# Performance work log

Measured on AMD Instinct MI355X. Metric: run time of the kernel, lower is better.

The kernel has to match this reference:

```python
import jax, jax.numpy as jnp
import numpy as np

B, C, H, W = 32, 256, 56, 56
O, K = 512, 3


def setup_inputs() -> dict:
    key = jax.random.key(0)
    kx, kw = jax.random.split(key)
    x = jax.random.normal(kx, (B, C, H, W), dtype=jnp.float32)
    # Ternary weight stored as two disjoint boolean masks of shape (C*K*K, O),
    # matching the torch buffer layout: weight.view(O, C*K*K).t().
    u = jax.random.uniform(kw, (C * K * K, O))
    pos_weight = u < 0.45
    neg_weight = u > 0.55
    return {"x": x, "pos_weight": pos_weight, "neg_weight": neg_weight}


def reference(x, pos_weight, neg_weight):
    # pos/neg masks: (C*K*K, O) bool, disjoint. The torch module computes
    # sum(unfold(x) where pos) - sum(unfold(x) where neg) over the C*K*K axis
    # per output channel, i.e. a conv with ternary weight in {-1, 0, +1}.
    b, c, h, w = x.shape
    ckk, o = pos_weight.shape
    k = int(round((ckk // c) ** 0.5))  # kernel size (square)
    wt = pos_weight.astype(x.dtype) - neg_weight.astype(x.dtype)  # (C*K*K, O)
    # torch unfold orders the patch axis as (C, kh, kw); weight came from
    # view(O, C*K*K).t(), so transposing back gives OIHW layout directly.
    wt = wt.T.reshape(o, c, k, k)
    pad = (k - 1) // 2  # 'same' padding (output reshaped to (b, O, h, w))
    out = jax.lax.conv_general_dilated(
        x, wt,
        window_strides=(1, 1),
        padding=[(pad, pad), (pad, pad)],
        dimension_numbers=("NCHW", "OIHW", "NCHW"),
    )
    return out  # (b, O, h, w)
```

## Files before the change

kernel.cpp:

```cpp
#include <hip/hip_runtime.h>
#include <hip/hip_bf16.h>

#define BB 32
#define CC 256
#define HH 56
#define WW 56
#define OO 512
#define CKK 2304

#define PROWS 58
#define PPITCH 64
#define PSLICE (PROWS * PPITCH)

#define NY 4
#define NX 28
#define NTILE 112
#define BPITCH 40

typedef __bf16 bf16x8 __attribute__((ext_vector_type(8)));
typedef float  f32x4  __attribute__((ext_vector_type(4)));
typedef unsigned short u16x8 __attribute__((ext_vector_type(8)));

#define WT_OFF 4096
#define XP_OFF (WT_OFF + (size_t)OO * CKK * 2)

__global__ void detect_bool_width(const unsigned int* __restrict__ pos,
                                  unsigned int* __restrict__ flag) {
    unsigned int v = 0;
    for (int i = threadIdx.x; i < 16384; i += 256) v |= pos[i];
    __shared__ unsigned int red;
    if (threadIdx.x == 0) red = 0u;
    __syncthreads();
    if (v > 1u) atomicOr(&red, 1u);
    __syncthreads();
    if (threadIdx.x == 0) *flag = red;
}

__global__ __launch_bounds__(256) void decode_w(
    const void* __restrict__ posv, const void* __restrict__ negv,
    const unsigned int* __restrict__ flag,
    unsigned short* __restrict__ wt) {
    __shared__ unsigned short lds[64][65];
    int blk = blockIdx.x;
    int ot  = blk & 7;
    int khw = (blk >> 3) % 9;
    int ct  = blk / 72;
    int o0 = ot * 64, c0 = ct * 64;
    int t = threadIdx.x;
    int o_l = t & 63, row4 = t >> 6;
    bool bytes = (*flag != 0u);
#pragma unroll
    for (int r = 0; r < 16; ++r) {
        int c_l = row4 + r * 4;
        long k = (long)(c0 + c_l) * 9 + khw;
        long idx = k * OO + o0 + o_l;
        int p, q;
        if (bytes) { p = ((const unsigned char*)posv)[idx];
                     q = ((const unsigned char*)negv)[idx]; }
        else       { p = ((const int*)posv)[idx];
                     q = ((const int*)negv)[idx]; }
        lds[c_l][o_l] = p ? 0x3F80u : (q ? 0xBF80u : 0u);
    }
    __syncthreads();
#pragma unroll
    for (int r = 0; r < 16; ++r) {
        int o_r = row4 + r * 4;
        int kcol = t & 63;
        wt[(size_t)(o0 + o_r) * CKK + khw * 256 + c0 + kcol] = lds[kcol][o_r];
    }
}

__global__ __launch_bounds__(256) void pad_x(const float* __restrict__ x,
                                             unsigned short* __restrict__ xp) {
    int bc = blockIdx.x;
    const float* xs = x + (size_t)bc * (HH * WW);
    unsigned short* xd = xp + (size_t)bc * PSLICE;
    for (int i = threadIdx.x; i < PSLICE; i += 256) {
        int xx = i & 63, yy = i >> 6;
        float v = 0.f;
        if (yy >= 1 && yy <= HH && xx >= 1 && xx <= WW)
            v = xs[(yy - 1) * WW + xx - 1];
        __hip_bfloat16 h = __float2bfloat16(v);
        xd[i] = *(unsigned short*)&h;
    }
}

__global__ __launch_bounds__(256, 2) void conv_mfma(
    const unsigned short* __restrict__ xp,
    const unsigned short* __restrict__ wt,
    float* __restrict__ out) {
    __shared__ __align__(16) unsigned short Bs[NTILE * BPITCH];

    int t = threadIdx.x;
    int w = t >> 6, lane = t & 63, lm = lane & 15, lq = lane >> 4;

    int gn = blockIdx.x;
    int obase = blockIdx.y << 8;
    int b = gn / 28;
    int rem = gn - b * 28;
    int y0 = (rem >> 1) * NY;
    int x0 = (rem & 1) * NX;

    int sn = t % NTILE;
    int ch = t / NTILE;
    bool active = (t < 2 * NTILE);
    int ny = sn / NX, nx = sn - (sn / NX) * NX;
    const unsigned short* xbase =
        xp + (size_t)(b * CC) * PSLICE + (y0 + ny) * PPITCH + (x0 + nx);
    int woff = sn * BPITCH + ch * 16;

    const unsigned short* abase =
        wt + (size_t)(obase + w * 64 + lm) * CKK + lq * 8;

    f32x4 acc[4][7];
#pragma unroll
    for (int i = 0; i < 4; ++i)
#pragma unroll
        for (int j = 0; j < 7; ++j) acc[i][j] = (f32x4){0.f, 0.f, 0.f, 0.f};

    for (int s = 0; s < 72; ++s) {
        int khw = s >> 3;
        int kh = khw / 3, kw = khw - kh * 3;
        int c0 = (s & 7) << 5;

        __syncthreads();
        if (active) {
            const unsigned short* src =
                xbase + (size_t)(c0 + ch * 16) * PSLICE + kh * PPITCH + kw;
            u16x8 v0, v1;
#pragma unroll
            for (int j = 0; j < 8; ++j) v0[j] = src[j * PSLICE];
#pragma unroll
            for (int j = 0; j < 8; ++j) v1[j] = src[(j + 8) * PSLICE];
            *(u16x8*)&Bs[woff] = v0;
            *(u16x8*)&Bs[woff + 8] = v1;
        }
        __syncthreads();

        bf16x8 af[4];
#pragma unroll
        for (int mt = 0; mt < 4; ++mt)
            af[mt] = *(const bf16x8*)(abase + (size_t)mt * 16 * CKK + s * 32);

#pragma unroll
        for (int nt = 0; nt < 7; ++nt) {
            bf16x8 bfr = *(const bf16x8*)&Bs[(nt * 16 + lm) * BPITCH + lq * 8];
#pragma unroll
            for (int mt = 0; mt < 4; ++mt)
                acc[mt][nt] = __builtin_amdgcn_mfma_f32_16x16x32_bf16(
                    af[mt], bfr, acc[mt][nt], 0, 0, 0);
        }
    }

    int orow0 = obase + w * 64 + lq * 4;
#pragma unroll
    for (int mt = 0; mt < 4; ++mt) {
#pragma unroll
        for (int nt = 0; nt < 7; ++nt) {
            int nl = nt * 16 + lm;
            int nyy = nl / NX, nxx = nl - nyy * NX;
            size_t base =
                ((size_t)(b * OO + orow0 + mt * 16) * HH + (y0 + nyy)) * WW +
                (x0 + nxx);
#pragma unroll
            for (int r = 0; r < 4; ++r)
                out[base + (size_t)r * HH * WW] = acc[mt][nt][r];
        }
    }
}

extern "C" void kernel_launch(void* const* d_in, const int* in_sizes, int n_in,
                              void* d_out, int out_size, void* d_ws, size_t ws_size,
                              hipStream_t stream) {
    const float* x   = (const float*)d_in[0];
    const void*  pos = d_in[1];
    const void*  neg = d_in[2];
    float* out = (float*)d_out;

    unsigned int* flag = (unsigned int*)d_ws;
    unsigned short* wt = (unsigned short*)((char*)d_ws + WT_OFF);
    unsigned short* xpad = (unsigned short*)((char*)d_ws + XP_OFF);

    detect_bool_width<<<1, 256, 0, stream>>>((const unsigned int*)pos, flag);
    decode_w<<<288, 256, 0, stream>>>(pos, neg, flag, wt);
    pad_x<<<BB * CC, 256, 0, stream>>>(x, xpad);
    conv_mfma<<<dim3(896, 2), 256, 0, stream>>>(xpad, wt, out);
}
```

Baseline: 759.5 us.

## Switch to channels-last padded input with halo tile staged via direct global-to-LDS loads

The padded input moves from per-channel planes (NCHW) to a channels-last layout (B, 58, 58, C), and the weights are reordered so each 32-channel chunk holds all 9 kernel taps together. The conv kernel now stages one 6x30-pixel halo tile of 32 channels into LDS once, using global_load_lds, and reuses it for all 9 taps. The old kernel gathered strided scalars from global memory for every tap. Staging is double-buffered so the next chunk's copy overlaps the MFMA work, and blocks are remapped so the two output-channel halves of a tile run close together for L2 reuse. The pad kernel gains an LDS transpose, and the conv kernel uses more registers (12 A fragments) and 32KB of LDS.

Result: faster. 616.3 us (-18.9%).

```diff
diff --git a/kernel.cpp b/kernel.cpp
--- a/kernel.cpp
+++ b/kernel.cpp
@@ -8,18 +8,19 @@
 #define OO 512
 #define CKK 2304
 
-#define PROWS 58
-#define PPITCH 64
-#define PSLICE (PROWS * PPITCH)
+#define XR 58
+#define XC 58
+#define XPIX (XR * XC)
 
 #define NY 4
 #define NX 28
 #define NTILE 112
-#define BPITCH 40
+#define TPC 30
+#define TPIX 180
+#define BUFB 16384
 
 typedef __bf16 bf16x8 __attribute__((ext_vector_type(8)));
 typedef float  f32x4  __attribute__((ext_vector_type(4)));
-typedef unsigned short u16x8 __attribute__((ext_vector_type(8)));
 
 #define WT_OFF 4096
 #define XP_OFF (WT_OFF + (size_t)OO * CKK * 2)
@@ -65,23 +66,44 @@
 #pragma unroll
     for (int r = 0; r < 16; ++r) {
         int o_r = row4 + r * 4;
-        int kcol = t & 63;
-        wt[(size_t)(o0 + o_r) * CKK + khw * 256 + c0 + kcol] = lds[kcol][o_r];
+        int c = c0 + (t & 63);
+        wt[(size_t)(o0 + o_r) * CKK + (c >> 5) * 288 + khw * 32 + (c & 31)] =
+            lds[t & 63][o_r];
     }
 }
 
 __global__ __launch_bounds__(256) void pad_x(const float* __restrict__ x,
                                              unsigned short* __restrict__ xp) {
-    int bc = blockIdx.x;
-    const float* xs = x + (size_t)bc * (HH * WW);
-    unsigned short* xd = xp + (size_t)bc * PSLICE;
-    for (int i = threadIdx.x; i < PSLICE; i += 256) {
-        int xx = i & 63, yy = i >> 6;
-        float v = 0.f;
-        if (yy >= 1 && yy <= HH && xx >= 1 && xx <= WW)
-            v = xs[(yy - 1) * WW + xx - 1];
-        __hip_bfloat16 h = __float2bfloat16(v);
-        xd[i] = *(unsigned short*)&h;
+    int blk = blockIdx.x;
+    int b = blk / XR, y = blk - b * XR;
+    int t = threadIdx.x;
+    unsigned short* rowp = xp + ((size_t)b * XPIX + (size_t)y * XC) * CC;
+    if (y == 0 || y == XR - 1) {
+        uint4 z = {0, 0, 0, 0};
+        for (int i = t; i < XC * CC / 8; i += 256) ((uint4*)rowp)[i] = z;
+        return;
+    }
+    __shared__ float lds[WW][65];
+    for (int cb = 0; cb < 4; ++cb) {
+        if (cb) __syncthreads();
+#pragma unroll
+        for (int i = 0; i < 14; ++i) {
+            int idx = i * 256 + t;
+            int cl = idx / WW, xx = idx - cl * WW;
+            lds[xx][cl] =
+                x[(((size_t)b * CC + cb * 64 + cl) * HH + (y - 1)) * WW + xx];
+        }
+        __syncthreads();
+#pragma unroll
+        for (int i = 0; i < 15; ++i) {
+            int idx = i * 256 + t;
+            if (idx < XC * 64) {
+                int xx = idx >> 6, cl = idx & 63;
+                float v = (xx == 0 || xx == XC - 1) ? 0.f : lds[xx - 1][cl];
+                __hip_bfloat16 h = __float2bfloat16(v);
+                rowp[(size_t)xx * CC + cb * 64 + cl] = *(unsigned short*)&h;
+            }
+        }
     }
 }
 
@@ -89,28 +111,44 @@
     const unsigned short* __restrict__ xp,
     const unsigned short* __restrict__ wt,
     float* __restrict__ out) {
-    __shared__ __align__(16) unsigned short Bs[NTILE * BPITCH];
+    __shared__ __align__(1024) unsigned short Bs[2 * BUFB / 2];
 
     int t = threadIdx.x;
     int w = t >> 6, lane = t & 63, lm = lane & 15, lq = lane >> 4;
 
-    int gn = blockIdx.x;
-    int obase = blockIdx.y << 8;
+    int bx = blockIdx.x;
+    int mb = (bx >> 3) & 1;
+    int gn = ((bx >> 4) << 3) | (bx & 7);
     int b = gn / 28;
     int rem = gn - b * 28;
-    int y0 = (rem >> 1) * NY;
+    int y0 = (rem >> 1) << 2;
     int x0 = (rem & 1) * NX;
 
-    int sn = t % NTILE;
-    int ch = t / NTILE;
-    bool active = (t < 2 * NTILE);
-    int ny = sn / NX, nx = sn - (sn / NX) * NX;
-    const unsigned short* xbase =
-        xp + (size_t)(b * CC) * PSLICE + (y0 + ny) * PPITCH + (x0 + nx);
-    int woff = sn * BPITCH + ch * 16;
-
-    const unsigned short* abase =
-        wt + (size_t)(obase + w * 64 + lm) * CKK + lq * 8;
+    int bofs[7];
+#pragma unroll
+    for (int nt = 0; nt < 7; ++nt) {
+        int n = nt * 16 + lm;
+        int ny = n / NX, nx = n - (n / NX) * NX;
+        bofs[nt] = (ny * TPC + nx) * 64 + lq * 16;
+    }
+
+    const unsigned short* gsrc[3];
+    int useg[3];
+#pragma unroll
+    for (int i = 0; i < 3; ++i) {
+        int u = (w * 3 + i) * 64 + lane;
+        useg[i] = u;
+        int pix = u >> 2, quad = u & 3;
+        int py = pix / TPC, px = pix - py * TPC;
+        gsrc[i] = xp + ((size_t)b * XPIX + (y0 + py) * XC + (x0 + px)) * CC +
+                  quad * 8;
+    }
+    int ldsseg = (w * 3) * 1024;
+
+    const unsigned short* aptr[4];
+#pragma unroll
+    for (int mt = 0; mt < 4; ++mt)
+        aptr[mt] = wt + (size_t)(mb * 256 + w * 64 + mt * 16 + lm) * CKK + lq * 8;
 
     f32x4 acc[4][7];
 #pragma unroll
@@ -118,50 +156,80 @@
 #pragma unroll
         for (int j = 0; j < 7; ++j) acc[i][j] = (f32x4){0.f, 0.f, 0.f, 0.f};
 
-    for (int s = 0; s < 72; ++s) {
-        int khw = s >> 3;
-        int kh = khw / 3, kw = khw - kh * 3;
-        int c0 = (s & 7) << 5;
-
+    bf16x8 af[12];
+
+#define STAGE(CHOFF, POFS)                                                     \
+    {                                                                          \
+        _Pragma("unroll") for (int i = 0; i < 3; ++i) {                        \
+            if (useg[i] < TPIX * 4)                                            \
+                __builtin_amdgcn_global_load_lds(                              \
+                    (const __attribute__((address_space(1))) void*)(gsrc[i] +  \
+                                                                    (CHOFF)),  \
+                    (__attribute__((address_space(3))) void*)((char*)Bs +      \
+                                                              (POFS) + ldsseg +\
+                                                              i * 1024),       \
+                    16, 0, 0);                                                 \
+        }                                                                      \
+    }
+
+#define LOADA(CHEL, G)                                                         \
+    {                                                                          \
+        _Pragma("unroll") for (int j = 0; j < 3; ++j)                          \
+            _Pragma("unroll") for (int mt = 0; mt < 4; ++mt)                   \
+                af[j * 4 + mt] = *(const bf16x8*)(aptr[mt] + (CHEL) +          \
+                                                  ((G) * 3 + j) * 32);         \
+    }
+
+#define GRP(G, POFS)                                                           \
+    {                                                                          \
+        _Pragma("unroll") for (int j = 0; j < 3; ++j) {                        \
+            const int khw = (G) * 3 + j;                                       \
+            const int kh = khw / 3, kw = khw - kh * 3;                         \
+            _Pragma("unroll") for (int nt = 0; nt < 7; ++nt) {                 \
+                bf16x8 bfr = *(const bf16x8*)((char*)Bs + (POFS) +             \
+                                              (kh * TPC + kw) * 64 + bofs[nt]);\
+                _Pragma("unroll") for (int mt = 0; mt < 4; ++mt)               \
+                    acc[mt][nt] = __builtin_amdgcn_mfma_f32_16x16x32_bf16(     \
+                        af[j * 4 + mt], bfr, acc[mt][nt], 0, 0, 0);            \
+            }                                                                  \
+        }                                                                      \
+    }
+
+    STAGE(0, 0);
+    LOADA(0, 0);
+    for (int it = 0; it < 4; ++it) {
         __syncthreads();
-        if (active) {
-            const unsigned short* src =
-                xbase + (size_t)(c0 + ch * 16) * PSLICE + kh * PPITCH + kw;
-            u16x8 v0, v1;
-#pragma unroll
-            for (int j = 0; j < 8; ++j) v0[j] = src[j * PSLICE];
-#pragma unroll
-            for (int j = 0; j < 8; ++j) v1[j] = src[(j + 8) * PSLICE];
-            *(u16x8*)&Bs[woff] = v0;
-            *(u16x8*)&Bs[woff + 8] = v1;
-        }
+        STAGE(32, BUFB);
+        GRP(0, 0);
+        LOADA(0, 1);  GRP(1, 0);
+        LOADA(0, 2);  GRP(2, 0);
+        LOADA(288, 0);
         __syncthreads();
-
-        bf16x8 af[4];
-#pragma unroll
-        for (int mt = 0; mt < 4; ++mt)
-            af[mt] = *(const bf16x8*)(abase + (size_t)mt * 16 * CKK + s * 32);
-
+        if (it < 3) STAGE(64, 0);
+        GRP(0, BUFB);
+        LOADA(288, 1); GRP(1, BUFB);
+        LOADA(288, 2); GRP(2, BUFB);
+        if (it < 3) {
+#pragma unroll
+            for (int mt = 0; mt < 4; ++mt) aptr[mt] += 576;
+#pragma unroll
+            for (int i = 0; i < 3; ++i) gsrc[i] += 64;
+            LOADA(0, 0);
+        }
+    }
+#undef STAGE
+#undef LOADA
+#undef GRP
+
+#pragma unroll
+    for (int mt = 0; mt < 4; ++mt) {
+        int o = mb * 256 + w * 64 + mt * 16 + lq * 4;
 #pragma unroll
         for (int nt = 0; nt < 7; ++nt) {
-            bf16x8 bfr = *(const bf16x8*)&Bs[(nt * 16 + lm) * BPITCH + lq * 8];
-#pragma unroll
-            for (int mt = 0; mt < 4; ++mt)
-                acc[mt][nt] = __builtin_amdgcn_mfma_f32_16x16x32_bf16(
-                    af[mt], bfr, acc[mt][nt], 0, 0, 0);
-        }
-    }
-
-    int orow0 = obase + w * 64 + lq * 4;
-#pragma unroll
-    for (int mt = 0; mt < 4; ++mt) {
-#pragma unroll
-        for (int nt = 0; nt < 7; ++nt) {
-            int nl = nt * 16 + lm;
-            int nyy = nl / NX, nxx = nl - nyy * NX;
+            int n = nt * 16 + lm;
+            int ny = n / NX, nx = n - (n / NX) * NX;
             size_t base =
-                ((size_t)(b * OO + orow0 + mt * 16) * HH + (y0 + nyy)) * WW +
-                (x0 + nxx);
+                (((size_t)b * OO + o) * HH + (y0 + ny)) * WW + (x0 + nx);
 #pragma unroll
             for (int r = 0; r < 4; ++r)
                 out[base + (size_t)r * HH * WW] = acc[mt][nt][r];
@@ -183,6 +251,6 @@
 
     detect_bool_width<<<1, 256, 0, stream>>>((const unsigned int*)pos, flag);
     decode_w<<<288, 256, 0, stream>>>(pos, neg, flag, wt);
-    pad_x<<<BB * CC, 256, 0, stream>>>(x, xpad);
-    conv_mfma<<<dim3(896, 2), 256, 0, stream>>>(xpad, wt, out);
-}
+    pad_x<<<BB * XR, 256, 0, stream>>>(x, xpad);
+    conv_mfma<<<dim3(1792), 256, 0, stream>>>(xpad, wt, out);
+}
```
